# Kernel optimization log

Hardware: AMD Instinct MI355X
Metric: run time of the kernel (lower is better)

## Reference

```python
import jax, jax.numpy as jnp
import numpy as np

ALPHA = 0.5
B = 4096
K = 8192


def setup_inputs() -> dict:
    key = jax.random.key(0)
    k1, k2 = jax.random.split(key)
    outputs = jax.random.normal(k1, (B, K), dtype=jnp.float32)
    labels = jax.random.randint(k2, (B,), 0, K)
    targets = jax.nn.one_hot(labels, K, dtype=jnp.float32)
    S = jnp.eye(K, dtype=jnp.float32)          # soft-label matrix (state)
    S_t = jnp.zeros((K, K), dtype=jnp.float32)  # running stats (state)
    count = jnp.zeros((K, 1), dtype=jnp.float32)
    return {"outputs": outputs, "targets": targets, "S": S, "S_t": S_t, "count": count}


def reference(outputs, targets, S, S_t, count):
    # loss path
    ls = jax.nn.log_softmax(outputs, axis=1)          # [B, K]
    bsz = outputs.shape[0]
    target_label = jnp.argmax(targets, axis=1)        # [B]
    prediction = jnp.argmax(outputs, axis=1)          # [B]
    soft_targets = S[target_label]                    # [B, K] gather
    ce_hard = -(ls * targets).sum() / bsz
    ce_soft = -(ls * soft_targets).sum() / bsz
    loss = ALPHA * ce_hard + (1.0 - ALPHA) * ce_soft

    # stats accumulation (the original python for-loop, as one fused scatter-add)
    probs = jax.nn.softmax(jax.lax.stop_gradient(outputs), axis=1)  # [B, K]
    correct = (prediction == target_label).astype(probs.dtype)      # [B]
    S_t_new = S_t + jax.ops.segment_sum(probs * correct[:, None], target_label, num_segments=K)
    count_new = count + jax.ops.segment_sum(correct, target_label, num_segments=K)[:, None]
    return loss, S_t_new, count_new
```

## Files before the change

### kernel.cpp

```cpp
#include <hip/hip_runtime.h>
#include <math.h>

#define K 8192
#define BROWS 4096
#define ALPHA 0.5f

typedef float f4u __attribute__((ext_vector_type(4), aligned(4)));

__device__ __forceinline__ void argmax_combine(float& v, int& i, float v2, int i2){
  if (v2 > v || (v2 == v && i2 < i)) { v = v2; i = i2; }
}

__global__ __launch_bounds__(256) void row_stats_kernel(
    const float* __restrict__ outputs,
    const float* __restrict__ targets,
    const float* __restrict__ S,
    float* __restrict__ rowloss,
    int*   __restrict__ rowtl,
    int*   __restrict__ rowcorrect,
    float* __restrict__ rowm,
    float* __restrict__ rowinvZ)
{
  __shared__ float xs[K];
  __shared__ float s_v[2][4]; __shared__ int s_i[2][4];
  __shared__ float s_m; __shared__ int s_pred; __shared__ int s_tl;
  __shared__ float s_sums[4][5];

  const int b = blockIdx.x;
  const int t = threadIdx.x;
  const int lane = t & 63;
  const int wid  = t >> 6;
  float4* xs4 = (float4*)xs;

  const float4* orow = (const float4*)(outputs + (size_t)b * K);
  float4 xv[8];
#pragma unroll
  for (int i = 0; i < 8; ++i) xv[i] = orow[i*256 + t];

  float mv = -INFINITY; int mi = 0x7fffffff;
#pragma unroll
  for (int i = 0; i < 8; ++i){
    xs4[i*256 + t] = xv[i];
    const float xc[4] = {xv[i].x, xv[i].y, xv[i].z, xv[i].w};
#pragma unroll
    for (int c = 0; c < 4; ++c)
      argmax_combine(mv, mi, xc[c], i*1024 + t*4 + c);
  }

  const float4* trow = (const float4*)(targets + (size_t)b * K);
  float4 tvv[8];
#pragma unroll
  for (int i = 0; i < 8; ++i) tvv[i] = trow[i*256 + t];

  float tv = -INFINITY; int ti = 0x7fffffff;
  float d_hard = 0.f, s_hard = 0.f;
#pragma unroll
  for (int i = 0; i < 8; ++i){
    const float xc[4] = {xv[i].x, xv[i].y, xv[i].z, xv[i].w};
    const float tc[4] = {tvv[i].x, tvv[i].y, tvv[i].z, tvv[i].w};
#pragma unroll
    for (int c = 0; c < 4; ++c){
      d_hard += xc[c] * tc[c];
      s_hard += tc[c];
      argmax_combine(tv, ti, tc[c], i*1024 + t*4 + c);
    }
  }

#pragma unroll
  for (int off = 32; off; off >>= 1){
    float v2 = __shfl_down(mv, off, 64); int i2 = __shfl_down(mi, off, 64);
    argmax_combine(mv, mi, v2, i2);
    v2 = __shfl_down(tv, off, 64); i2 = __shfl_down(ti, off, 64);
    argmax_combine(tv, ti, v2, i2);
  }
  if (lane == 0){ s_v[0][wid]=mv; s_i[0][wid]=mi; s_v[1][wid]=tv; s_i[1][wid]=ti; }
  __syncthreads();
  if (t == 0){
    float av=s_v[0][0]; int ai=s_i[0][0];
    float bv=s_v[1][0]; int bi=s_i[1][0];
#pragma unroll
    for (int w=1; w<4; ++w){
      argmax_combine(av, ai, s_v[0][w], s_i[0][w]);
      argmax_combine(bv, bi, s_v[1][w], s_i[1][w]);
    }
    s_m = av; s_pred = ai; s_tl = bi;
  }
  __syncthreads();
  const float m  = s_m;
  const int   tl = s_tl;

  const float4* srow = (const float4*)(S + (size_t)tl * K);
  float4 svv[8];
#pragma unroll
  for (int i = 0; i < 8; ++i) svv[i] = srow[i*256 + t];

  float se = 0.f, d_soft = 0.f, s_soft = 0.f;
#pragma unroll
  for (int i = 0; i < 8; ++i){
    float4 xr = xs4[i*256 + t];
    const float xc[4] = {xr.x, xr.y, xr.z, xr.w};
    const float sc[4] = {svv[i].x, svv[i].y, svv[i].z, svv[i].w};
#pragma unroll
    for (int c = 0; c < 4; ++c){
      se     += expf(xc[c] - m);
      d_soft += xc[c] * sc[c];
      s_soft += sc[c];
    }
  }

  float sums[5] = {d_hard, s_hard, se, d_soft, s_soft};
#pragma unroll
  for (int off = 32; off; off >>= 1){
#pragma unroll
    for (int j = 0; j < 5; ++j) sums[j] += __shfl_down(sums[j], off, 64);
  }
  if (lane == 0){
#pragma unroll
    for (int j = 0; j < 5; ++j) s_sums[wid][j] = sums[j];
  }
  __syncthreads();
  if (t == 0){
    float tot[5];
#pragma unroll
    for (int j=0;j<5;++j)
      tot[j] = s_sums[0][j]+s_sums[1][j]+s_sums[2][j]+s_sums[3][j];
    float Z = tot[2];
    float logZ = logf(Z);
    float ceh = -(tot[0] - (m + logZ) * tot[1]);
    float ces = -(tot[3] - (m + logZ) * tot[4]);
    rowloss[b]    = (ALPHA * ceh + (1.0f - ALPHA) * ces) * (1.0f / (float)BROWS);
    rowtl[b]      = tl;
    rowcorrect[b] = (s_pred == tl) ? 1 : 0;
    rowm[b]       = m;
    rowinvZ[b]    = 1.0f / Z;
  }
}

__global__ __launch_bounds__(256) void copy_st_kernel(const float* __restrict__ src,
                                                      float* __restrict__ dst){
  const f4u*  s4 = (const f4u*)(src + 3);
  float4*     d4 = (float4*)(dst + 3);
  const size_t n4     = 16777215UL;
  const size_t stride = 2097152UL;
  const size_t i = (size_t)blockIdx.x * 256 + threadIdx.x;

  if (i != stride - 1){
    float4 v[8];
#pragma unroll
    for (int k = 0; k < 8; ++k){
      f4u u = s4[i + (size_t)k * stride];
      v[k] = *(const float4*)&u;
    }
#pragma unroll
    for (int k = 0; k < 8; ++k)
      d4[i + (size_t)k * stride] = v[k];
  } else {
    float4 v[7];
#pragma unroll
    for (int k = 0; k < 7; ++k){
      f4u u = s4[i + (size_t)k * stride];
      v[k] = *(const float4*)&u;
    }
#pragma unroll
    for (int k = 0; k < 7; ++k)
      d4[i + (size_t)k * stride] = v[k];
    dst[0] = src[0]; dst[1] = src[1]; dst[2] = src[2];
    dst[67108863] = src[67108863];
  }
}

__global__ __launch_bounds__(256) void tail_kernel(const float* __restrict__ outputs,
    const int* __restrict__ rowtl, const int* __restrict__ rowcorrect,
    const float* __restrict__ rowm, const float* __restrict__ rowinvZ,
    const float* __restrict__ rowloss, const float* __restrict__ count,
    float* __restrict__ out_loss, float* __restrict__ out_St,
    float* __restrict__ out_count){
  const int b = blockIdx.x;
  const int t = threadIdx.x;
  if (b == BROWS){
    float s = 0.f;
    for (int i = t; i < BROWS; i += 256) s += rowloss[i];
#pragma unroll
    for (int off = 32; off; off >>= 1) s += __shfl_down(s, off, 64);
    __shared__ float sh[4];
    if ((t & 63) == 0) sh[t >> 6] = s;
    __syncthreads();
    if (t == 0) out_loss[0] = sh[0] + sh[1] + sh[2] + sh[3];
    for (int i = t; i < K; i += 256) out_count[i] = count[i];
    return;
  }
  if (!rowcorrect[b]) return;
  const int tl = rowtl[b];
  const float m = rowm[b], invZ = rowinvZ[b];
  const float* orow = outputs + (size_t)b * K;
  float* drow = out_St + (size_t)tl * K;
  for (int k = t; k < K; k += 256)
    atomicAdd(&drow[k], expf(orow[k] - m) * invZ);
  if (t == 0) atomicAdd(&out_count[tl], 1.0f);
}

extern "C" void kernel_launch(void* const* d_in, const int* in_sizes, int n_in,
                              void* d_out, int out_size, void* d_ws, size_t ws_size,
                              hipStream_t stream) {
  const float* outputs = (const float*)d_in[0];
  const float* targets = (const float*)d_in[1];
  const float* S       = (const float*)d_in[2];
  const float* S_t     = (const float*)d_in[3];
  const float* count   = (const float*)d_in[4];

  float* out       = (float*)d_out;
  float* out_loss  = out;
  float* out_St    = out + 1;
  float* out_count = out + 1 + (size_t)K * K;

  float* rowloss    = (float*)d_ws;
  float* rowm       = rowloss + BROWS;
  float* rowinvZ    = rowm + BROWS;
  int*   rowtl      = (int*)(rowinvZ + BROWS);
  int*   rowcorrect = rowtl + BROWS;

  hipLaunchKernelGGL(row_stats_kernel, dim3(BROWS), dim3(256), 0, stream,
                     outputs, targets, S, rowloss, rowtl, rowcorrect, rowm, rowinvZ);
  hipLaunchKernelGGL(copy_st_kernel, dim3(8192), dim3(256), 0, stream, S_t, out_St);
  hipLaunchKernelGGL(tail_kernel, dim3(BROWS + 1), dim3(256), 0, stream,
                     outputs, rowtl, rowcorrect, rowm, rowinvZ, rowloss, count,
                     out_loss, out_St, out_count);
}
```

Baseline: 744.3 us.

## Fuse S_t copy into row-stats kernel via interleaved block roles

```diff
diff --git a/kernel.cpp b/kernel.cpp
--- a/kernel.cpp
+++ b/kernel.cpp
@@ -11,10 +11,12 @@
   if (v2 > v || (v2 == v && i2 < i)) { v = v2; i = i2; }
 }
 
-__global__ __launch_bounds__(256) void row_stats_kernel(
+__global__ __launch_bounds__(256, 4) void fused_kernel(
     const float* __restrict__ outputs,
     const float* __restrict__ targets,
     const float* __restrict__ S,
+    const float* __restrict__ S_t,
+    float* __restrict__ out_St,
     float* __restrict__ rowloss,
     int*   __restrict__ rowtl,
     int*   __restrict__ rowcorrect,
@@ -26,8 +28,43 @@
   __shared__ float s_m; __shared__ int s_pred; __shared__ int s_tl;
   __shared__ float s_sums[4][5];
 
-  const int b = blockIdx.x;
-  const int t = threadIdx.x;
+  const int bb = blockIdx.x;
+  const int t  = threadIdx.x;
+  const int r  = bb % 3;
+
+  if (r != 0){
+    const int c = (bb / 3) * 2 + (r - 1);
+    const f4u* s4 = (const f4u*)(S_t + 3);
+    float4*    d4 = (float4*)(out_St + 3);
+    const size_t base = (size_t)c * 2048 + t;
+    if (c != 8191){
+      float4 v[8];
+#pragma unroll
+      for (int k = 0; k < 8; ++k){
+        f4u u = s4[base + (size_t)k * 256];
+        v[k] = *(const float4*)&u;
+      }
+#pragma unroll
+      for (int k = 0; k < 8; ++k)
+        d4[base + (size_t)k * 256] = v[k];
+    } else {
+#pragma unroll
+      for (int k = 0; k < 8; ++k){
+        size_t idx = base + (size_t)k * 256;
+        if (idx < 16777215UL){
+          f4u u = s4[idx];
+          d4[idx] = *(const float4*)&u;
+        }
+      }
+      if (t == 255){
+        out_St[0] = S_t[0]; out_St[1] = S_t[1]; out_St[2] = S_t[2];
+        out_St[67108863] = S_t[67108863];
+      }
+    }
+    return;
+  }
+
+  const int b = bb / 3;
   const int lane = t & 63;
   const int wid  = t >> 6;
   float4* xs4 = (float4*)xs;
@@ -136,39 +173,6 @@
   }
 }
 
-__global__ __launch_bounds__(256) void copy_st_kernel(const float* __restrict__ src,
-                                                      float* __restrict__ dst){
-  const f4u*  s4 = (const f4u*)(src + 3);
-  float4*     d4 = (float4*)(dst + 3);
-  const size_t n4     = 16777215UL;
-  const size_t stride = 2097152UL;
-  const size_t i = (size_t)blockIdx.x * 256 + threadIdx.x;
-
-  if (i != stride - 1){
-    float4 v[8];
-#pragma unroll
-    for (int k = 0; k < 8; ++k){
-      f4u u = s4[i + (size_t)k * stride];
-      v[k] = *(const float4*)&u;
-    }
-#pragma unroll
-    for (int k = 0; k < 8; ++k)
-      d4[i + (size_t)k * stride] = v[k];
-  } else {
-    float4 v[7];
-#pragma unroll
-    for (int k = 0; k < 7; ++k){
-      f4u u = s4[i + (size_t)k * stride];
-      v[k] = *(const float4*)&u;
-    }
-#pragma unroll
-    for (int k = 0; k < 7; ++k)
-      d4[i + (size_t)k * stride] = v[k];
-    dst[0] = src[0]; dst[1] = src[1]; dst[2] = src[2];
-    dst[67108863] = src[67108863];
-  }
-}
-
 __global__ __launch_bounds__(256) void tail_kernel(const float* __restrict__ outputs,
     const int* __restrict__ rowtl, const int* __restrict__ rowcorrect,
     const float* __restrict__ rowm, const float* __restrict__ rowinvZ,
@@ -219,9 +223,9 @@
   int*   rowtl      = (int*)(rowinvZ + BROWS);
   int*   rowcorrect = rowtl + BROWS;
 
-  hipLaunchKernelGGL(row_stats_kernel, dim3(BROWS), dim3(256), 0, stream,
-                     outputs, targets, S, rowloss, rowtl, rowcorrect, rowm, rowinvZ);
-  hipLaunchKernelGGL(copy_st_kernel, dim3(8192), dim3(256), 0, stream, S_t, out_St);
+  hipLaunchKernelGGL(fused_kernel, dim3(3 * BROWS), dim3(256), 0, stream,
+                     outputs, targets, S, S_t, out_St,
+                     rowloss, rowtl, rowcorrect, rowm, rowinvZ);
   hipLaunchKernelGGL(tail_kernel, dim3(BROWS + 1), dim3(256), 0, stream,
                      outputs, rowtl, rowcorrect, rowm, rowinvZ, rowloss, count,
                      out_loss, out_St, out_count);
```

Measured after the change: 733.9 us. About the same (-1.4%).
